# Performance work log

Hardware: AMD Instinct MI355X
Metric: run time of the kernel (lower is better)

## Reference

```python
import jax, jax.numpy as jnp
import numpy as np

B, T, C = 4, 2048, 2048
H, D, L = 16, 128, 512


def _rope(x, cos, sin):
    # x: [B, T, H, D]; cos/sin: [T, D//2]; consecutive-pair complex rotation
    x2 = x.reshape(*x.shape[:-1], -1, 2)
    x0, x1 = x2[..., 0], x2[..., 1]
    c = cos[None, :, None, :]
    s = sin[None, :, None, :]
    o0 = x0 * c - x1 * s
    o1 = x0 * s + x1 * c
    return jnp.stack([o0, o1], axis=-1).reshape(x.shape)


def setup_inputs() -> dict:
    key = jax.random.key(0)
    ks = jax.random.split(key, 8)
    x = jax.random.normal(ks[0], (B, T, C), dtype=jnp.float32)
    # rotary table, theta = 10000
    inv_freq = 1.0 / (10000.0 ** (np.arange(0, D, 2, dtype=np.float32) / D))
    ang = np.outer(np.arange(T, dtype=np.float32), inv_freq)
    freqs_cos = jnp.asarray(np.cos(ang), dtype=jnp.float32)
    freqs_sin = jnp.asarray(np.sin(ang), dtype=jnp.float32)
    sc = 0.02
    wq = sc * jax.random.normal(ks[1], (H * D, C), dtype=jnp.float32)
    wkv_down = sc * jax.random.normal(ks[2], (L, C), dtype=jnp.float32)
    wk_up = sc * jax.random.normal(ks[3], (D, L), dtype=jnp.float32)
    wv_up = sc * jax.random.normal(ks[4], (D, L), dtype=jnp.float32)
    wo = sc * jax.random.normal(ks[5], (C, H * D), dtype=jnp.float32)
    return {"x": x, "freqs_cos": freqs_cos, "freqs_sin": freqs_sin,
            "wq": wq, "wkv_down": wkv_down, "wk_up": wk_up,
            "wv_up": wv_up, "wo": wo}


def reference(x, freqs_cos, freqs_sin, wq, wkv_down, wk_up, wv_up, wo):
    Bc, Tc, Cc = x.shape
    # query projection -> [B, T, H, D]
    q = jnp.einsum('btc,ec->bte', x, wq).reshape(Bc, Tc, H, D)
    # shared latent KV: [B, T, L]
    kv_latent = jnp.einsum('btc,lc->btl', x, wkv_down)
    # up-project to single shared head: [B, T, D]
    k = jnp.einsum('btl,dl->btd', kv_latent, wk_up)
    v = jnp.einsum('btl,dl->btd', kv_latent, wv_up)
    # RoPE on q (per head) and k (single shared head)
    q = _rope(q, freqs_cos, freqs_sin)
    k = _rope(k[:, :, None, :], freqs_cos, freqs_sin)[:, :, 0, :]
    # causal SDPA; k/v are shared across heads (MLA) so avoid expanding them
    scale = 1.0 / jnp.sqrt(jnp.asarray(D, dtype=x.dtype))
    scores = jnp.einsum('bthd,bsd->bhts', q, k) * scale  # [B, H, T, S]
    causal = jnp.tril(jnp.ones((Tc, Tc), dtype=bool))
    scores = jnp.where(causal[None, None, :, :], scores, jnp.finfo(x.dtype).min)
    probs = jax.nn.softmax(scores, axis=-1)
    y = jnp.einsum('bhts,bsd->bthd', probs, v).reshape(Bc, Tc, H * D)
    return jnp.einsum('bte,ce->btc', y, wo)
```

## Files before the change

kernel.cpp:

```cpp
#include <hip/hip_runtime.h>
#include <hip/hip_bf16.h>
#include <cstddef>

#define BB 4
#define TT 2048
#define CC 2048
#define HH 16
#define DD 128
#define LL 512

typedef _Float16 f16;
typedef f16 f16x2 __attribute__((ext_vector_type(2)));
typedef f16 f16x4 __attribute__((ext_vector_type(4)));
typedef f16 f16x8 __attribute__((ext_vector_type(8)));
typedef float f32x4 __attribute__((ext_vector_type(4)));

__device__ __forceinline__ void async_load16(void* lptr, const void* gptr) {
  __builtin_amdgcn_global_load_lds(
      (const __attribute__((address_space(1))) unsigned int*)gptr,
      (__attribute__((address_space(3))) unsigned int*)lptr, 16, 0, 0);
}

template <int EPI>
__global__ __launch_bounds__(512, 2) void mla_gemm_256(
    const f16* __restrict__ A, const f16* __restrict__ B,
    void* __restrict__ Cv, int M, int N, int K,
    const float* __restrict__ cosb, const float* __restrict__ sinb) {
  __shared__ __align__(16) f16 smem[2][2][256 * 64];

  const int tid = threadIdx.x;
  const int lane = tid & 63;
  const int w = tid >> 6;
  const int lnm = lane & 15, quad = lane >> 4;
  const int wm = w >> 2, wn = w & 3;

  const int nwg = gridDim.x;
  const int bid0 = blockIdx.x;
  const int q8 = nwg >> 3, r8 = nwg & 7;
  const int xcd = bid0 & 7, lid = bid0 >> 3;
  const int wg =
      (xcd < r8 ? xcd * (q8 + 1) : r8 * (q8 + 1) + (xcd - r8) * q8) + lid;
  const int ntc = N >> 8;
  const int m0 = (wg / ntc) * 256;
  const int n0 = (wg % ntc) * 256;

  const int srow = tid >> 3;
  const int sch = (tid & 7) ^ ((tid >> 3) & 7);
  const f16* Ag = A + (size_t)(m0 + srow) * K + sch * 8;
  const f16* Bg = B + (size_t)(n0 + srow) * K + sch * 8;

  auto stage = [&](int bi, int k0, int h) {
    const int mat = h >> 1;
    const int rb = (h & 1) * 128;
    const f16* g = (mat ? Bg : Ag) + (size_t)rb * K + k0;
    f16* l = &smem[bi][mat][rb * 64 + tid * 8];
    async_load16(l, g);
    async_load16(l + 4096, g + (size_t)64 * K);
  };

  const int rx8 = lnm & 7;
  auto rdA = [&](const f16* Ab, int i, int ks) -> f16x8 {
    return *(const f16x8*)&Ab[(wm * 128 + i * 16 + lnm) * 64 +
                              (((ks * 4 + quad) ^ rx8) * 8)];
  };
  auto rdB = [&](const f16* Bb, int j, int ks) -> f16x8 {
    return *(const f16x8*)&Bb[(wn * 64 + j * 16 + lnm) * 64 +
                              (((ks * 4 + quad) ^ rx8) * 8)];
  };

  f32x4 acc[8][4] = {};

  const int NT = K >> 6;

  stage(0, 0, 0);
  stage(0, 0, 1);
  stage(0, 0, 2);
  stage(0, 0, 3);
  stage(1, 64, 0);
  asm volatile("s_waitcnt vmcnt(2)" ::: "memory");
  __builtin_amdgcn_s_barrier();

  for (int t = 0; t < NT; ++t) {
    const int bi = t & 1;
    const f16* Ab = smem[bi][0];
    const f16* Bb = smem[bi][1];
    const int k1 = (t + 1 < NT ? t + 1 : t) << 6;
    const int k2 = (t + 2 < NT ? t + 2 : t) << 6;

    f16x8 Ar[4][2], Br[2][2];

#pragma unroll
    for (int i = 0; i < 4; i++)
#pragma unroll
      for (int ks = 0; ks < 2; ks++) Ar[i][ks] = rdA(Ab, i, ks);
#pragma unroll
    for (int j = 0; j < 2; j++)
#pragma unroll
      for (int ks = 0; ks < 2; ks++) Br[j][ks] = rdB(Bb, j, ks);
    stage(bi ^ 1, k1, 1);
    __builtin_amdgcn_s_barrier();
    asm volatile("s_waitcnt lgkmcnt(0)" ::: "memory");
    __builtin_amdgcn_s_setprio(1);
#pragma unroll
    for (int i = 0; i < 4; i++)
#pragma unroll
      for (int j = 0; j < 2; j++)
#pragma unroll
        for (int ks = 0; ks < 2; ks++)
          acc[i][j] = __builtin_amdgcn_mfma_f32_16x16x32_f16(
              Ar[i][ks], Br[j][ks], acc[i][j], 0, 0, 0);
    __builtin_amdgcn_s_setprio(0);
    __builtin_amdgcn_s_barrier();

#pragma unroll
    for (int j = 0; j < 2; j++)
#pragma unroll
      for (int ks = 0; ks < 2; ks++) Br[j][ks] = rdB(Bb, 2 + j, ks);
    stage(bi ^ 1, k1, 2);
    __builtin_amdgcn_s_barrier();
    asm volatile("s_waitcnt lgkmcnt(0)" ::: "memory");
    __builtin_amdgcn_s_setprio(1);
#pragma unroll
    for (int i = 0; i < 4; i++)
#pragma unroll
      for (int j = 0; j < 2; j++)
#pragma unroll
        for (int ks = 0; ks < 2; ks++)
          acc[i][2 + j] = __builtin_amdgcn_mfma_f32_16x16x32_f16(
              Ar[i][ks], Br[j][ks], acc[i][2 + j], 0, 0, 0);
    __builtin_amdgcn_s_setprio(0);
    __builtin_amdgcn_s_barrier();

#pragma unroll
    for (int i = 0; i < 4; i++)
#pragma unroll
      for (int ks = 0; ks < 2; ks++) Ar[i][ks] = rdA(Ab, 4 + i, ks);
    stage(bi ^ 1, k1, 3);
    __builtin_amdgcn_s_barrier();
    asm volatile("s_waitcnt lgkmcnt(0)" ::: "memory");
    __builtin_amdgcn_s_setprio(1);
#pragma unroll
    for (int i = 0; i < 4; i++)
#pragma unroll
      for (int j = 0; j < 2; j++)
#pragma unroll
        for (int ks = 0; ks < 2; ks++)
          acc[4 + i][2 + j] = __builtin_amdgcn_mfma_f32_16x16x32_f16(
              Ar[i][ks], Br[j][ks], acc[4 + i][2 + j], 0, 0, 0);
    __builtin_amdgcn_s_setprio(0);
    __builtin_amdgcn_s_barrier();

#pragma unroll
    for (int j = 0; j < 2; j++)
#pragma unroll
      for (int ks = 0; ks < 2; ks++) Br[j][ks] = rdB(Bb, j, ks);
    stage(bi, k2, 0);
    __builtin_amdgcn_s_barrier();
    asm volatile("s_waitcnt lgkmcnt(0)" ::: "memory");
    __builtin_amdgcn_s_setprio(1);
#pragma unroll
    for (int i = 0; i < 4; i++)
#pragma unroll
      for (int j = 0; j < 2; j++)
#pragma unroll
        for (int ks = 0; ks < 2; ks++)
          acc[4 + i][j] = __builtin_amdgcn_mfma_f32_16x16x32_f16(
              Ar[i][ks], Br[j][ks], acc[4 + i][j], 0, 0, 0);
    __builtin_amdgcn_s_setprio(0);
    asm volatile("s_waitcnt vmcnt(2)" ::: "memory");
    __builtin_amdgcn_s_barrier();
  }

  asm volatile("s_waitcnt vmcnt(0)" ::: "memory");

  if constexpr (EPI == 0) {
    float* C = (float*)Cv;
#pragma unroll
    for (int i = 0; i < 8; i++)
#pragma unroll
      for (int r = 0; r < 4; r++) {
        float* crow = C + (size_t)(m0 + wm * 128 + i * 16 + quad * 4 + r) * N +
                      n0 + wn * 64 + lnm;
#pragma unroll
        for (int j = 0; j < 4; j++) crow[j * 16] = acc[i][j][r];
      }
  } else {
    f16* C = (f16*)Cv;
    const float SCLQ = 0.1275174280f;
#pragma unroll
    for (int i = 0; i < 8; i++)
#pragma unroll
      for (int r = 0; r < 4; r++) {
        const int m = m0 + wm * 128 + i * 16 + quad * 4 + r;
        const int t = m & (TT - 1);
#pragma unroll
        for (int j = 0; j < 4; j++) {
          const int col = n0 + wn * 64 + j * 16 + lnm;
          float v = acc[i][j][r];
          float u = __shfl_xor(v, 1, 64);
          const int fi = (col & (DD - 1)) >> 1;
          const float ct = cosb[t * (DD / 2) + fi];
          const float st2 = sinb[t * (DD / 2) + fi];
          const float o =
              (lnm & 1) ? (u * st2 + v * ct) : (v * ct - u * st2);
          C[(size_t)m * N + col] = (f16)(o * SCLQ);
        }
      }
  }
}

__global__ __launch_bounds__(256) void mla_gemm_mfma_h(
    const f16* __restrict__ A, const f16* __restrict__ B,
    f16* __restrict__ C, int M, int N, int K) {
  __shared__ f16 As[128 * 32];
  __shared__ f16 Bs[128 * 32];

  const int tid = threadIdx.x;
  const int lane = tid & 63;
  const int w = tid >> 6;
  const int lnm = lane & 15, quad = lane >> 4;
  const int wm = w >> 1, wn = w & 1;
  const int m0 = blockIdx.y * 128;
  const int n0 = blockIdx.x * 128;

  const int srow = tid >> 2;
  const int skoff = (tid & 3) * 8;

  f32x4 acc[4][4] = {};

  for (int k0 = 0; k0 < K; k0 += 32) {
    const f16* ag = A + (size_t)(m0 + srow) * K + k0 + skoff;
    const f16* bg = B + (size_t)(n0 + srow) * K + k0 + skoff;
    async_load16(&As[(size_t)tid * 8], ag);
    async_load16(&As[(size_t)(256 + tid) * 8], ag + (size_t)64 * K);
    async_load16(&Bs[(size_t)tid * 8], bg);
    async_load16(&Bs[(size_t)(256 + tid) * 8], bg + (size_t)64 * K);
    __syncthreads();

    f16x8 af[4], bf[4];
#pragma unroll
    for (int i = 0; i < 4; i++)
      af[i] = *(const f16x8*)&As[(wm * 64 + i * 16 + lnm) * 32 + quad * 8];
#pragma unroll
    for (int j = 0; j < 4; j++)
      bf[j] = *(const f16x8*)&Bs[(wn * 64 + j * 16 + lnm) * 32 + quad * 8];
#pragma unroll
    for (int i = 0; i < 4; i++)
#pragma unroll
      for (int j = 0; j < 4; j++)
        acc[i][j] = __builtin_amdgcn_mfma_f32_16x16x32_f16(af[i], bf[j],
                                                           acc[i][j], 0, 0, 0);
    __syncthreads();
  }

#pragma unroll
  for (int i = 0; i < 4; i++)
#pragma unroll
    for (int r = 0; r < 4; r++) {
      f16* crow = C + (size_t)(m0 + wm * 64 + i * 16 + quad * 4 + r) * N +
                  n0 + wn * 64 + lnm;
#pragma unroll
      for (int j = 0; j < 4; j++) crow[j * 16] = (f16)acc[i][j][r];
    }
}

__global__ __launch_bounds__(256) void mla_gemm_upkv(
    const f16* __restrict__ A, const f16* __restrict__ B,
    f16* __restrict__ khp, f16* __restrict__ vtp,
    const float* __restrict__ cosb, const float* __restrict__ sinb) {
  const int NN = 256, KK = 512;
  __shared__ f16 As[128 * 32];
  __shared__ f16 Bs[128 * 32];

  const int tid = threadIdx.x;
  const int lane = tid & 63;
  const int w = tid >> 6;
  const int lnm = lane & 15, quad = lane >> 4;
  const int wm = w >> 1, wn = w & 1;
  const int m0 = blockIdx.y * 128;
  const int n0 = blockIdx.x * 128;

  const int srow = tid >> 2;
  const int skoff = (tid & 3) * 8;

  f32x4 acc[4][4] = {};

  for (int k0 = 0; k0 < KK; k0 += 32) {
    const f16* ag = A + (size_t)(m0 + srow) * KK + k0 + skoff;
    const f16* bg = B + (size_t)(n0 + srow) * KK + k0 + skoff;
    async_load16(&As[(size_t)tid * 8], ag);
    async_load16(&As[(size_t)(256 + tid) * 8], ag + (size_t)64 * KK);
    async_load16(&Bs[(size_t)tid * 8], bg);
    async_load16(&Bs[(size_t)(256 + tid) * 8], bg + (size_t)64 * KK);
    __syncthreads();

    f16x8 af[4], bf[4];
#pragma unroll
    for (int i = 0; i < 4; i++)
      af[i] = *(const f16x8*)&As[(wm * 64 + i * 16 + lnm) * 32 + quad * 8];
#pragma unroll
    for (int j = 0; j < 4; j++)
      bf[j] = *(const f16x8*)&Bs[(wn * 64 + j * 16 + lnm) * 32 + quad * 8];
#pragma unroll
    for (int i = 0; i < 4; i++)
#pragma unroll
      for (int j = 0; j < 4; j++)
        acc[i][j] = __builtin_amdgcn_mfma_f32_16x16x32_f16(af[i], bf[j],
                                                           acc[i][j], 0, 0, 0);
    __syncthreads();
  }

  const bool isv = (n0 != 0);
#pragma unroll
  for (int i = 0; i < 4; i++)
#pragma unroll
    for (int r = 0; r < 4; r++) {
      const int m = m0 + wm * 64 + i * 16 + quad * 4 + r;
      const int b = m >> 11, t = m & (TT - 1);
      const int st = t >> 6, s = t & 63;
      if (!isv) {
        f16* tb = khp + (size_t)(b * 32 + st) * 8192;
#pragma unroll
        for (int j = 0; j < 4; j++) {
          const int n = wn * 64 + j * 16 + lnm;
          float v = acc[i][j][r];
          float u = __shfl_xor(v, 1, 64);
          const int fi = n >> 1;
          const float ct = cosb[t * 64 + fi];
          const float st2 = sinb[t * 64 + fi];
          const float o = (lnm & 1) ? (u * st2 + v * ct) : (v * ct - u * st2);
          tb[(n >> 3) * 512 + s * 8 + (n & 7)] = (f16)o;
        }
      } else {
        const int cq2 = ((s >> 5) << 2) | ((s >> 2) & 3);
        const int e = (((s >> 4) & 1) << 2) | (s & 3);
        f16* tb = vtp + (size_t)(b * 32 + st) * 8192 + cq2 * 1024 + e;
#pragma unroll
        for (int j = 0; j < 4; j++) {
          const int d = wn * 64 + j * 16 + lnm;
          tb[d * 8] = (f16)acc[i][j][r];
        }
      }
    }
}

#define CVT_C0 ((size_t)BB * TT * CC)
#define CVT_C1 (CVT_C0 + (size_t)CC * CC)
#define CVT_C2 (CVT_C1 + (size_t)LL * CC)
#define CVT_C3 (CVT_C2 + (size_t)DD * LL)
#define CVT_C4 (CVT_C3 + (size_t)DD * LL)
#define CVT_C5 (CVT_C4 + (size_t)CC * CC)
__global__ __launch_bounds__(256) void mla_cvt_all(
    const float* __restrict__ x, const float* __restrict__ wq,
    const float* __restrict__ wdn, const float* __restrict__ wku,
    const float* __restrict__ wvu, const float* __restrict__ wo,
    f16* __restrict__ dst) {
  size_t i4 = (size_t)blockIdx.x * 256 + threadIdx.x;
  if (i4 >= CVT_C5 / 4) return;
  size_t e = i4 * 4;
  const float* src;
  size_t off;
  if (e < CVT_C0) { src = x; off = e; }
  else if (e < CVT_C1) { src = wq; off = e - CVT_C0; }
  else if (e < CVT_C2) { src = wdn; off = e - CVT_C1; }
  else if (e < CVT_C3) { src = wku; off = e - CVT_C2; }
  else if (e < CVT_C4) { src = wvu; off = e - CVT_C3; }
  else { src = wo; off = e - CVT_C4; }
  float4 v = *(const float4*)&src[off];
  f16x4 r = {(f16)v.x, (f16)v.y, (f16)v.z, (f16)v.w};
  *(f16x4*)(dst + e) = r;
}

__global__ __launch_bounds__(512, 2) void mla_flash2(
    const f16* __restrict__ qh, const f16* __restrict__ khp,
    const f16* __restrict__ vtp, f16* __restrict__ y) {
  __shared__ __align__(16) f16 Ks[2][8192];
  __shared__ __align__(16) f16 Vs[2][8192];

  const int tid = threadIdx.x;
  const int lane = tid & 63;
  const int w = tid >> 6;
  const int lnm = lane & 15, quad = lane >> 4;

  const int bid = blockIdx.x;
  const int qt = (TT / 256 - 1) - (bid >> 6);
  const int bh = bid & 63;
  const int b = bh >> 4, h = bh & 15;
  const int q0b = qt * 256;
  const int q0 = q0b + w * 32;

  f16x8 qf[2][4];
#pragma unroll
  for (int qnb = 0; qnb < 2; qnb++) {
    const f16* qrow =
        qh + ((size_t)(b * TT + q0 + qnb * 16 + lnm) * HH + h) * DD;
#pragma unroll
    for (int c = 0; c < 4; c++)
      qf[qnb][c] = *(const f16x8*)(qrow + c * 32 + quad * 8);
  }

  f32x4 O[2][8] = {};
  f32x4 S[2][4];
  float l_acc[2] = {0.f, 0.f};

  const int nst = (q0b + 256) / 64;
  const int wmax = q0 + 31;
  const f16* kpb = khp + (size_t)b * 32 * 8192;
  const f16* vpb = vtp + (size_t)b * 32 * 8192;

  auto stageK = [&](int buf, int st) {
    const f16* g = kpb + (size_t)st * 8192 + (size_t)tid * 8;
    async_load16(&Ks[buf][(size_t)tid * 8], g);
    async_load16(&Ks[buf][(size_t)(512 + tid) * 8], g + 4096);
  };
  auto stageV = [&](int buf, int st) {
    const f16* g = vpb + (size_t)st * 8192 + (size_t)tid * 8;
    async_load16(&Vs[buf][(size_t)tid * 8], g);
    async_load16(&Vs[buf][(size_t)(512 + tid) * 8], g + 4096);
  };

  const int kbo = quad * 512 + lnm * 8;
  const int vbo = quad * 1024 + lnm * 8;

  auto qk = [&](const f16* Kbuf) {
    const f16* kl = Kbuf + kbo;
    const f32x4 z = {0.f, 0.f, 0.f, 0.f};
#pragma unroll
    for (int qnb = 0; qnb < 2; qnb++)
#pragma unroll
      for (int sb = 0; sb < 4; sb++) S[qnb][sb] = z;
#pragma unroll
    for (int sb = 0; sb < 4; sb++)
#pragma unroll
      for (int c = 0; c < 4; c++) {
        f16x8 ka = *(const f16x8*)&kl[c * 2048 + sb * 128];
        S[0][sb] = __builtin_amdgcn_mfma_f32_16x16x32_f16(ka, qf[0][c],
                                                          S[0][sb], 0, 0, 0);
        S[1][sb] = __builtin_amdgcn_mfma_f32_16x16x32_f16(ka, qf[1][c],
                                                          S[1][sb], 0, 0, 0);
      }
  };

  stageK(0, 0);
  stageV(0, 0);
  __syncthreads();
  stageK(1, 1);
  qk(Ks[0]);
  __syncthreads();

  for (int st = 0; st < nst; st++) {
    const int cur = st & 1, nxt = cur ^ 1;
    const int s0 = st * 64;
    stageK(cur, st + 2 < nst ? st + 2 : nst - 1);
    stageV(nxt, st + 1 < nst ? st + 1 : nst - 1);

    const bool act = (s0 <= wmax);
    f16x8 P8[2][2];
    if (act) {
      const bool domask = (s0 + 63 > q0);
      if (!domask) {
#pragma unroll
        for (int qnb = 0; qnb < 2; qnb++) {
          float lp = 0.f;
#pragma unroll
          for (int sb = 0; sb < 4; sb++)
#pragma unroll
            for (int j = 0; j < 4; j++) {
              float p = __builtin_amdgcn_exp2f(S[qnb][sb][j]);
              lp += p;
              P8[qnb][sb >> 1][(sb & 1) * 4 + j] = (f16)p;
            }
          l_acc[qnb] += lp;
        }
      } else {
#pragma unroll
        for (int qnb = 0; qnb < 2; qnb++) {
          const int m_abs = q0 + qnb * 16 + lnm;
          float lp = 0.f;
#pragma unroll
          for (int sb = 0; sb < 4; sb++) {
            const int srow = s0 + sb * 16 + quad * 4;
#pragma unroll
            for (int j = 0; j < 4; j++) {
              float p = __builtin_amdgcn_exp2f(S[qnb][sb][j]);
              if (srow + j > m_abs) p = 0.f;
              lp += p;
              P8[qnb][sb >> 1][(sb & 1) * 4 + j] = (f16)p;
            }
          }
          l_acc[qnb] += lp;
        }
      }
    }

    __builtin_amdgcn_s_setprio(1);
    if ((st + 1) * 64 <= wmax) qk(Ks[nxt]);

    if (act) {
      const f16* vl = &Vs[cur][vbo];
#pragma unroll
      for (int c = 0; c < 2; c++)
#pragma unroll
        for (int db = 0; db < 8; db++) {
          f16x8 vb = *(const f16x8*)&vl[c * 4096 + db * 128];
          O[0][db] = __builtin_amdgcn_mfma_f32_16x16x32_f16(P8[0][c], vb,
                                                            O[0][db], 0, 0, 0);
          O[1][db] = __builtin_amdgcn_mfma_f32_16x16x32_f16(P8[1][c], vb,
                                                            O[1][db], 0, 0, 0);
        }
    }
    __builtin_amdgcn_s_setprio(0);
    __syncthreads();
  }

#pragma unroll
  for (int qnb = 0; qnb < 2; qnb++) {
    float l = l_acc[qnb];
    l += __shfl_xor(l, 16, 64);
    l += __shfl_xor(l, 32, 64);
    l_acc[qnb] = l;
  }

#pragma unroll
  for (int qnb = 0; qnb < 2; qnb++) {
    float linv[4];
#pragma unroll
    for (int r = 0; r < 4; r++)
      linv[r] = 1.f / __shfl(l_acc[qnb], quad * 4 + r, 64);
#pragma unroll
    for (int db = 0; db < 8; db++)
#pragma unroll
      for (int r = 0; r < 4; r++) {
        size_t off =
            ((size_t)(b * TT + q0 + qnb * 16 + quad * 4 + r) * HH + h) * DD +
            db * 16 + lnm;
        y[off] = (f16)(O[qnb][db][r] * linv[r]);
      }
  }
}

extern "C" void kernel_launch(void* const* d_in, const int* in_sizes, int n_in,
                              void* d_out, int out_size, void* d_ws,
                              size_t ws_size, hipStream_t stream) {
  const float* x      = (const float*)d_in[0];
  const float* fcos   = (const float*)d_in[1];
  const float* fsin   = (const float*)d_in[2];
  const float* wq     = (const float*)d_in[3];
  const float* wkv_dn = (const float*)d_in[4];
  const float* wk_up  = (const float*)d_in[5];
  const float* wv_up  = (const float*)d_in[6];
  const float* wo     = (const float*)d_in[7];
  float* out = (float*)d_out;

  const int M = BB * TT;

  float* ws = (float*)d_ws;
  float* qbuf   = ws;
  f16*   xh     = (f16*)(qbuf + (size_t)M * CC);
  f16*   wqh    = xh + (size_t)M * CC;
  f16*   wdownh = wqh + (size_t)CC * CC;
  f16*   wkvuph = wdownh + (size_t)LL * CC;
  f16*   woh    = wkvuph + (size_t)256 * LL;
  f16*   kvh    = woh + (size_t)CC * CC;
  f16*   khp    = kvh + (size_t)M * LL;
  f16*   vtp    = khp + (size_t)M * DD;
  f16*   qh     = (f16*)qbuf;
  f16*   yh     = qh + (size_t)M * CC;

  {
    size_t total4 = CVT_C5 / 4;
    mla_cvt_all<<<(unsigned)((total4 + 255) / 256), dim3(256), 0, stream>>>(
        x, wq, wkv_dn, wk_up, wv_up, wo, xh);
  }

  mla_gemm_256<1><<<dim3((M / 256) * (CC / 256)), dim3(512), 0, stream>>>(
      xh, wqh, qh, M, CC, CC, fcos, fsin);

  mla_gemm_mfma_h<<<dim3(LL / 128, M / 128), dim3(256), 0, stream>>>(
      xh, wdownh, kvh, M, LL, CC);

  mla_gemm_upkv<<<dim3(2, M / 128), dim3(256), 0, stream>>>(
      kvh, wkvuph, khp, vtp, fcos, fsin);

  mla_flash2<<<dim3(BB * HH * (TT / 256)), dim3(512), 0, stream>>>(
      qh, khp, vtp, yh);

  mla_gemm_256<0><<<dim3((M / 256) * (CC / 256)), dim3(512), 0, stream>>>(
      yh, woh, out, M, CC, CC, nullptr, nullptr);
}
```

Before: 432.1 us.

## Shrink flash attention blocks to 128 queries and simplify K/V staging pipeline

The flash attention kernel now uses 256-thread blocks covering 128 queries each, doubling the grid, and targets three blocks per CU. The software pipeline that computed the next tile's QK scores ahead of time is removed, and V becomes single-buffered, loaded after a second per-iteration barrier. The goal is finer causal load balancing and lower LDS and register use to raise occupancy. In exchange the kernel gives up the QK/PV overlap inside each block, adds an extra barrier per step, and each block loads K/V tiles for fewer queries, so K/V traffic per query rises.

```diff
diff --git a/kernel.cpp b/kernel.cpp
--- a/kernel.cpp
+++ b/kernel.cpp
@@ -269,6 +269,7 @@
     f16* __restrict__ khp, f16* __restrict__ vtp,
     const float* __restrict__ cosb, const float* __restrict__ sinb) {
   const int NN = 256, KK = 512;
+  (void)NN;
   __shared__ f16 As[128 * 32];
   __shared__ f16 Bs[128 * 32];
 
@@ -371,11 +372,11 @@
   *(f16x4*)(dst + e) = r;
 }
 
-__global__ __launch_bounds__(512, 2) void mla_flash2(
+__global__ __launch_bounds__(256, 3) void mla_flash2(
     const f16* __restrict__ qh, const f16* __restrict__ khp,
     const f16* __restrict__ vtp, f16* __restrict__ y) {
   __shared__ __align__(16) f16 Ks[2][8192];
-  __shared__ __align__(16) f16 Vs[2][8192];
+  __shared__ __align__(16) f16 Vs[8192];
 
   const int tid = threadIdx.x;
   const int lane = tid & 63;
@@ -383,10 +384,10 @@
   const int lnm = lane & 15, quad = lane >> 4;
 
   const int bid = blockIdx.x;
-  const int qt = (TT / 256 - 1) - (bid >> 6);
+  const int qt = (TT / 128 - 1) - (bid >> 6);
   const int bh = bid & 63;
   const int b = bh >> 4, h = bh & 15;
-  const int q0b = qt * 256;
+  const int q0b = qt * 128;
   const int q0 = q0b + w * 32;
 
   f16x8 qf[2][4];
@@ -400,63 +401,56 @@
   }
 
   f32x4 O[2][8] = {};
-  f32x4 S[2][4];
   float l_acc[2] = {0.f, 0.f};
 
-  const int nst = (q0b + 256) / 64;
+  const int nst = (q0b + 128) / 64;
   const int wmax = q0 + 31;
   const f16* kpb = khp + (size_t)b * 32 * 8192;
   const f16* vpb = vtp + (size_t)b * 32 * 8192;
 
   auto stageK = [&](int buf, int st) {
     const f16* g = kpb + (size_t)st * 8192 + (size_t)tid * 8;
-    async_load16(&Ks[buf][(size_t)tid * 8], g);
-    async_load16(&Ks[buf][(size_t)(512 + tid) * 8], g + 4096);
+#pragma unroll
+    for (int i = 0; i < 4; i++)
+      async_load16(&Ks[buf][(size_t)(i * 256 + tid) * 8], g + i * 2048);
   };
-  auto stageV = [&](int buf, int st) {
+  auto stageV = [&](int st) {
     const f16* g = vpb + (size_t)st * 8192 + (size_t)tid * 8;
-    async_load16(&Vs[buf][(size_t)tid * 8], g);
-    async_load16(&Vs[buf][(size_t)(512 + tid) * 8], g + 4096);
+#pragma unroll
+    for (int i = 0; i < 4; i++)
+      async_load16(&Vs[(size_t)(i * 256 + tid) * 8], g + i * 2048);
   };
 
   const int kbo = quad * 512 + lnm * 8;
   const int vbo = quad * 1024 + lnm * 8;
 
-  auto qk = [&](const f16* Kbuf) {
-    const f16* kl = Kbuf + kbo;
-    const f32x4 z = {0.f, 0.f, 0.f, 0.f};
-#pragma unroll
-    for (int qnb = 0; qnb < 2; qnb++)
-#pragma unroll
-      for (int sb = 0; sb < 4; sb++) S[qnb][sb] = z;
-#pragma unroll
-    for (int sb = 0; sb < 4; sb++)
-#pragma unroll
-      for (int c = 0; c < 4; c++) {
-        f16x8 ka = *(const f16x8*)&kl[c * 2048 + sb * 128];
-        S[0][sb] = __builtin_amdgcn_mfma_f32_16x16x32_f16(ka, qf[0][c],
-                                                          S[0][sb], 0, 0, 0);
-        S[1][sb] = __builtin_amdgcn_mfma_f32_16x16x32_f16(ka, qf[1][c],
-                                                          S[1][sb], 0, 0, 0);
-      }
-  };
-
   stageK(0, 0);
-  stageV(0, 0);
+  stageV(0);
   __syncthreads();
-  stageK(1, 1);
-  qk(Ks[0]);
-  __syncthreads();
 
   for (int st = 0; st < nst; st++) {
-    const int cur = st & 1, nxt = cur ^ 1;
+    const int cur = st & 1;
     const int s0 = st * 64;
-    stageK(cur, st + 2 < nst ? st + 2 : nst - 1);
-    stageV(nxt, st + 1 < nst ? st + 1 : nst - 1);
+    if (st + 1 < nst) stageK(cur ^ 1, st + 1);
 
     const bool act = (s0 <= wmax);
     f16x8 P8[2][2];
     if (act) {
+      const f16* kl = &Ks[cur][kbo];
+      f32x4 S[2][4] = {};
+      __builtin_amdgcn_s_setprio(1);
+#pragma unroll
+      for (int sb = 0; sb < 4; sb++)
+#pragma unroll
+        for (int c = 0; c < 4; c++) {
+          f16x8 ka = *(const f16x8*)&kl[c * 2048 + sb * 128];
+          S[0][sb] = __builtin_amdgcn_mfma_f32_16x16x32_f16(ka, qf[0][c],
+                                                            S[0][sb], 0, 0, 0);
+          S[1][sb] = __builtin_amdgcn_mfma_f32_16x16x32_f16(ka, qf[1][c],
+                                                            S[1][sb], 0, 0, 0);
+        }
+      __builtin_amdgcn_s_setprio(0);
+
       const bool domask = (s0 + 63 > q0);
       if (!domask) {
 #pragma unroll
@@ -493,11 +487,11 @@
       }
     }
 
-    __builtin_amdgcn_s_setprio(1);
-    if ((st + 1) * 64 <= wmax) qk(Ks[nxt]);
+    __syncthreads();
 
     if (act) {
-      const f16* vl = &Vs[cur][vbo];
+      const f16* vl = &Vs[vbo];
+      __builtin_amdgcn_s_setprio(1);
 #pragma unroll
       for (int c = 0; c < 2; c++)
 #pragma unroll
@@ -508,9 +502,11 @@
           O[1][db] = __builtin_amdgcn_mfma_f32_16x16x32_f16(P8[1][c], vb,
                                                             O[1][db], 0, 0, 0);
         }
+      __builtin_amdgcn_s_setprio(0);
     }
-    __builtin_amdgcn_s_setprio(0);
+
     __syncthreads();
+    if (st + 1 < nst) stageV(st + 1);
   }
 
 #pragma unroll
@@ -582,7 +578,7 @@
   mla_gemm_upkv<<<dim3(2, M / 128), dim3(256), 0, stream>>>(
       kvh, wkvuph, khp, vtp, fcos, fsin);
 
-  mla_flash2<<<dim3(BB * HH * (TT / 256)), dim3(512), 0, stream>>>(
+  mla_flash2<<<dim3(BB * HH * (TT / 128)), dim3(256), 0, stream>>>(
       qh, khp, vtp, yh);
 
   mla_gemm_256<0><<<dim3((M / 256) * (CC / 256)), dim3(512), 0, stream>>>(
```

Result: faster. 417.3 us (-3.4%).
